# Performance work log

Hardware: AMD Instinct MI355X
Metric: run time of the kernel (lower is better)

## Reference

```python
import jax, jax.numpy as jnp
import numpy as np
import math

N_HEAD = 16
LATENT_RANK = 64

def setup_inputs() -> dict:
    key = jax.random.key(0)
    ks = jax.random.split(key, 8)
    B, T, C, H, R = 4, 2048, 1024, N_HEAD, LATENT_RANK
    std = 0.02
    return {
        "hidden_states": jax.random.normal(ks[0], (B, T, C), jnp.float32),
        "basis_w": jax.random.normal(ks[1], (R, C), jnp.float32) * std,
        "core": jax.random.normal(ks[2], (R, R), jnp.float32) * std,
        "head_residual": jax.random.normal(ks[3], (H, R, R), jnp.float32) * (std / 10.0),
        "v_w": jax.random.normal(ks[4], (C, C), jnp.float32) * std,
        "v_b": jnp.zeros((C,), jnp.float32),
        "o_w": jax.random.normal(ks[5], (C, C), jnp.float32) * std,
        "o_b": jnp.zeros((C,), jnp.float32),
    }

def reference(hidden_states, basis_w, core, head_residual, v_w, v_b, o_w, o_b):
    B, T, C = hidden_states.shape
    H = N_HEAD
    R = LATENT_RANK
    head_dim = C // H

    # latent projection: [B,T,R]
    latent = jnp.einsum('btc,rc->btr', hidden_states, basis_w)

    # symmetric core + centered per-head residual -> head matrices [H,R,R]
    core_sym = 0.5 * (core + core.T)
    centered = head_residual - head_residual.mean(axis=0, keepdims=True)
    head_mats = core_sym[None] / float(H) + centered

    # bilinear latent attention scores [B,H,T,T]
    lt = jnp.einsum('btr,hrs->bhts', latent, head_mats)  # fold Q-transform
    att = jnp.einsum('bhts,bus->bhtu', lt, latent) * (1.0 / math.sqrt(R))

    # causal mask + softmax
    causal = jnp.tril(jnp.ones((T, T), jnp.bool_))
    att = jnp.where(causal[None, None], att, jnp.float32(-jnp.inf))
    att = jax.nn.softmax(att, axis=-1)

    # value projection [B,H,T,head_dim]
    v = (hidden_states @ v_w.T + v_b).reshape(B, T, H, head_dim).transpose(0, 2, 1, 3)
    y = att @ v  # [B,H,T,head_dim]
    y = y.transpose(0, 2, 1, 3).reshape(B, T, C)
    y = y @ o_w.T + o_b
    return y
```

## Files before the change

### kernel.cpp

```cpp
#include <hip/hip_runtime.h>
#include <hip/hip_bf16.h>


#define N_HEAD 16
#define RANK 64

typedef __attribute__((ext_vector_type(8))) short bf16x8;
typedef __attribute__((ext_vector_type(4))) float f32x4;

__device__ __forceinline__ ushort f2b(float f) {
    unsigned u = __builtin_bit_cast(unsigned, f);
    u += 0x7fffu + ((u >> 16) & 1u);
    return (ushort)(u >> 16);
}

__device__ __forceinline__ int swz(int row, int col) {
    return (row << 6) | (col ^ ((row & 7) << 3));
}

__global__ void cvt_kernel(const float* __restrict__ src, ushort* __restrict__ dst, int n4) {
    int i = blockIdx.x * blockDim.x + threadIdx.x;
    if (i >= n4) return;
    float4 v = ((const float4*)src)[i];
    ushort4 o;
    o.x = f2b(v.x); o.y = f2b(v.y); o.z = f2b(v.z); o.w = f2b(v.w);
    ((ushort4*)dst)[i] = o;
}

__global__ void headmats_kernel(const float* __restrict__ core,
                                const float* __restrict__ resid,
                                ushort* __restrict__ hmT) {
    int idx = blockIdx.x * 256 + threadIdx.x;
    if (idx >= RANK * RANK) return;
    int r = idx >> 6, s = idx & 63;
    float mean = 0.f;
    for (int h = 0; h < N_HEAD; ++h) mean += resid[h * RANK * RANK + idx];
    mean *= (1.0f / N_HEAD);
    float cs = 0.5f * (core[r * RANK + s] + core[s * RANK + r]) * (1.0f / N_HEAD);
    for (int h = 0; h < N_HEAD; ++h) {
        float val = cs + resid[h * RANK * RANK + idx] - mean;
        hmT[h * RANK * RANK + s * RANK + r] = f2b(val);
    }
}

__global__ __launch_bounds__(256) void gemm_nt(
    const ushort* __restrict__ A, const ushort* __restrict__ W,
    const float* __restrict__ bias,
    float* __restrict__ outF, ushort* __restrict__ outB,
    int M, int N, int K,
    int zDivA, long long aStride, int zModW, long long wStride, long long oStride,
    int outVT)
{
    __shared__ ushort As[128 * 72];
    __shared__ ushort Ws[64 * 72];

    int z = blockIdx.z;
    A += (size_t)(z / zDivA) * aStride;
    W += (size_t)(z % zModW) * wStride;
    size_t obase = (size_t)z * oStride;

    int m0 = blockIdx.y * 128;
    int n0 = blockIdx.x * 64;
    int t = threadIdx.x;
    int wave = t >> 6, lane = t & 63;
    int wr = wave >> 1, wc = wave & 1;
    int g = lane >> 4, ln = lane & 15;

    f32x4 acc[4][2];
    for (int i = 0; i < 4; ++i)
        for (int j = 0; j < 2; ++j) acc[i][j] = (f32x4){0.f, 0.f, 0.f, 0.f};

    for (int k0 = 0; k0 < K; k0 += 64) {
        for (int q = 0; q < 4; ++q) {
            int e = (t + 256 * q) * 8;
            int row = e >> 6, col = e & 63;
            *(bf16x8*)&As[row * 72 + col] =
                *(const bf16x8*)(A + (size_t)(m0 + row) * K + k0 + col);
        }
        for (int q = 0; q < 2; ++q) {
            int e = (t + 256 * q) * 8;
            int row = e >> 6, col = e & 63;
            *(bf16x8*)&Ws[row * 72 + col] =
                *(const bf16x8*)(W + (size_t)(n0 + row) * K + k0 + col);
        }
        __syncthreads();
        for (int ks = 0; ks < 2; ++ks) {
            bf16x8 a[4], b[2];
            for (int fm = 0; fm < 4; ++fm)
                a[fm] = *(const bf16x8*)&As[(wr * 64 + fm * 16 + ln) * 72 + ks * 32 + 8 * g];
            for (int fn = 0; fn < 2; ++fn)
                b[fn] = *(const bf16x8*)&Ws[(wc * 32 + fn * 16 + ln) * 72 + ks * 32 + 8 * g];
            for (int fm = 0; fm < 4; ++fm)
                for (int fn = 0; fn < 2; ++fn)
                    acc[fm][fn] = __builtin_amdgcn_mfma_f32_16x16x32_bf16(
                        a[fm], b[fn], acc[fm][fn], 0, 0, 0);
        }
        __syncthreads();
    }

    if (outVT) {
        for (int fm = 0; fm < 4; ++fm)
            for (int fn = 0; fn < 2; ++fn) {
                int row = m0 + wr * 64 + fm * 16 + 4 * g;
                int col = n0 + wc * 32 + fn * 16 + ln;
                float bv = bias ? bias[col] : 0.f;
                ushort4 us;
                us.x = f2b(acc[fm][fn][0] + bv);
                us.y = f2b(acc[fm][fn][1] + bv);
                us.z = f2b(acc[fm][fn][2] + bv);
                us.w = f2b(acc[fm][fn][3] + bv);
                size_t off = ((size_t)(row >> 11) * 1024 + col) * 2048 + (row & 2047);
                *(ushort4*)(outB + off) = us;
            }
    } else {
        for (int fm = 0; fm < 4; ++fm)
            for (int fn = 0; fn < 2; ++fn)
                for (int r = 0; r < 4; ++r) {
                    int row = m0 + wr * 64 + fm * 16 + 4 * g + r;
                    int col = n0 + wc * 32 + fn * 16 + ln;
                    float val = acc[fm][fn][r];
                    if (bias) val += bias[col];
                    size_t o = obase + (size_t)row * N + col;
                    if (outF) outF[o] = val;
                    if (outB) outB[o] = f2b(val);
                }
    }
}

__global__ __launch_bounds__(256) void attn_kernel(
    const ushort* __restrict__ lt, const ushort* __restrict__ latent,
    const ushort* __restrict__ vT, ushort* __restrict__ y)
{
    const int T = 2048, C = 1024;
    __shared__ ushort Ps[4][32 * 64];

    int pq = blockIdx.x, h = blockIdx.y, b = blockIdx.z;
    int t = threadIdx.x, w = t >> 6, lane = t & 63;
    int g = lane >> 4, ln = lane & 15;

    const ushort* Kg = latent + (size_t)b * T * RANK;
    const ushort* Vg = vT + (size_t)(b * N_HEAD + h) * 64 * T;
    ushort* Pw = Ps[w];

    const float SCL = 0.125f * 1.44269504089f;
    const float THR = 11.5f;

    for (int pass = 0; pass < 2; ++pass) {
        int qt = pass ? (15 - pq) : pq;
        int qrow0 = qt * 128 + w * 32;

        const ushort* Qg = lt + ((size_t)(b * N_HEAD + h) * T + qrow0) * RANK;
        bf16x8 qa[2][2];
        for (int m = 0; m < 2; ++m)
            for (int ks = 0; ks < 2; ++ks)
                qa[m][ks] = *(const bf16x8*)(Qg + (size_t)(m * 16 + ln) * RANK + ks * 32 + 8 * g);

        float mr[2][4], lp[2][4];
        f32x4 o[2][4];
        for (int m = 0; m < 2; ++m)
            for (int r = 0; r < 4; ++r) { mr[m][r] = -INFINITY; lp[m][r] = 0.f; }
        for (int m = 0; m < 2; ++m)
            for (int fn = 0; fn < 4; ++fn) o[m][fn] = (f32x4){0.f, 0.f, 0.f, 0.f};

        int kmax = 2 * qt + 1;
        for (int kt = 0; kt <= kmax; ++kt) {
            f32x4 s[2][4];
            for (int m = 0; m < 2; ++m)
                for (int fn = 0; fn < 4; ++fn) s[m][fn] = (f32x4){0.f, 0.f, 0.f, 0.f};
            for (int ks = 0; ks < 2; ++ks) {
                bf16x8 kb[4];
                for (int fn = 0; fn < 4; ++fn)
                    kb[fn] = *(const bf16x8*)(Kg +
                        (size_t)(kt * 64 + fn * 16 + ln) * RANK + ks * 32 + 8 * g);
                for (int m = 0; m < 2; ++m)
                    for (int fn = 0; fn < 4; ++fn)
                        s[m][fn] = __builtin_amdgcn_mfma_f32_16x16x32_bf16(
                            qa[m][ks], kb[fn], s[m][fn], 0, 0, 0);
            }

            bf16x8 vb[2][4];
            for (int ks = 0; ks < 2; ++ks)
                for (int fn = 0; fn < 4; ++fn)
                    vb[ks][fn] = *(const bf16x8*)(Vg +
                        (size_t)(fn * 16 + ln) * T + kt * 64 + ks * 32 + 8 * g);

            float rm[2][4];
            for (int m = 0; m < 2; ++m) {
                for (int r = 0; r < 4; ++r) rm[m][r] = -INFINITY;
                int qb = qrow0 + m * 16 + 4 * g;
                if ((kt * 64 + 63) > (qrow0 + m * 16)) {
                    for (int fn = 0; fn < 4; ++fn) {
                        int key = kt * 64 + fn * 16 + ln;
                        for (int r = 0; r < 4; ++r) {
                            float sv = s[m][fn][r] * SCL;
                            if (key > qb + r) sv = -INFINITY;
                            s[m][fn][r] = sv;
                            rm[m][r] = fmaxf(rm[m][r], sv);
                        }
                    }
                } else {
                    for (int fn = 0; fn < 4; ++fn)
                        for (int r = 0; r < 4; ++r) {
                            float sv = s[m][fn][r] * SCL;
                            s[m][fn][r] = sv;
                            rm[m][r] = fmaxf(rm[m][r], sv);
                        }
                }
            }

            int need = 0;
            for (int m = 0; m < 2; ++m)
                for (int r = 0; r < 4; ++r) need |= (rm[m][r] > mr[m][r] + THR);
            if (__any(need)) {
                for (int off = 1; off < 16; off <<= 1)
                    for (int m = 0; m < 2; ++m)
                        for (int r = 0; r < 4; ++r)
                            rm[m][r] = fmaxf(rm[m][r], __shfl_xor(rm[m][r], off));
                for (int m = 0; m < 2; ++m)
                    for (int r = 0; r < 4; ++r) {
                        float nm = fmaxf(mr[m][r], rm[m][r]);
                        float al = exp2f(mr[m][r] - nm);
                        mr[m][r] = nm;
                        lp[m][r] *= al;
                        for (int fn = 0; fn < 4; ++fn) o[m][fn][r] *= al;
                    }
            }

            for (int m = 0; m < 2; ++m)
                for (int fn = 0; fn < 4; ++fn)
                    for (int r = 0; r < 4; ++r) {
                        float p = exp2f(s[m][fn][r] - mr[m][r]);
                        lp[m][r] += p;
                        Pw[swz(m * 16 + 4 * g + r, fn * 16 + ln)] = f2b(p);
                    }

            for (int ks = 0; ks < 2; ++ks) {
                bf16x8 pa[2];
                for (int m = 0; m < 2; ++m)
                    pa[m] = *(const bf16x8*)&Pw[swz(m * 16 + ln, ks * 32 + 8 * g)];
                for (int m = 0; m < 2; ++m)
                    for (int fn = 0; fn < 4; ++fn)
                        o[m][fn] = __builtin_amdgcn_mfma_f32_16x16x32_bf16(
                            pa[m], vb[ks][fn], o[m][fn], 0, 0, 0);
            }
        }

        for (int off = 1; off < 16; off <<= 1)
            for (int m = 0; m < 2; ++m)
                for (int r = 0; r < 4; ++r) lp[m][r] += __shfl_xor(lp[m][r], off);
        for (int m = 0; m < 2; ++m)
            for (int fn = 0; fn < 4; ++fn)
                for (int r = 0; r < 4; ++r) {
                    int row = qrow0 + m * 16 + 4 * g + r;
                    y[((size_t)b * T + row) * C + h * 64 + fn * 16 + ln] =
                        f2b(o[m][fn][r] / lp[m][r]);
                }
    }
}

extern "C" void kernel_launch(void* const* d_in, const int* in_sizes, int n_in,
                              void* d_out, int out_size, void* d_ws, size_t ws_size,
                              hipStream_t stream) {
    const float* hs    = (const float*)d_in[0];
    const float* basis = (const float*)d_in[1];
    const float* core  = (const float*)d_in[2];
    const float* resid = (const float*)d_in[3];
    const float* v_w   = (const float*)d_in[4];
    const float* v_b   = (const float*)d_in[5];
    const float* o_w   = (const float*)d_in[6];
    const float* o_b   = (const float*)d_in[7];
    float* out = (float*)d_out;

    const int B = 4, T = 2048, C = 1024, H = N_HEAD, R = RANK;
    const int M = B * T;

    char* ws = (char*)d_ws;
    ushort* hs_b    = (ushort*)(ws + 0);
    ushort* y_b     = hs_b;
    ushort* basis_b = (ushort*)(ws + 16777216);
    ushort* vw_b    = (ushort*)(ws + 16908288);
    ushort* ow_b    = (ushort*)(ws + 19005440);
    ushort* hm_b    = (ushort*)(ws + 21102592);
    ushort* lat_b   = (ushort*)(ws + 21233664);
    ushort* lt_b    = (ushort*)(ws + 22282240);
    ushort* vT_b    = (ushort*)(ws + 39059456);

    cvt_kernel<<<dim3(M * C / 4 / 256), 256, 0, stream>>>(hs, hs_b, M * C / 4);
    cvt_kernel<<<dim3(R * C / 4 / 256), 256, 0, stream>>>(basis, basis_b, R * C / 4);
    cvt_kernel<<<dim3(C * C / 4 / 256), 256, 0, stream>>>(v_w, vw_b, C * C / 4);
    cvt_kernel<<<dim3(C * C / 4 / 256), 256, 0, stream>>>(o_w, ow_b, C * C / 4);

    headmats_kernel<<<dim3(16), 256, 0, stream>>>(core, resid, hm_b);

    gemm_nt<<<dim3(1, M / 128, 1), 256, 0, stream>>>(
        hs_b, basis_b, nullptr, nullptr, lat_b, M, R, C, 1, 0, 1, 0, 0, 0);

    gemm_nt<<<dim3(C / 64, M / 128, 1), 256, 0, stream>>>(
        hs_b, vw_b, v_b, nullptr, vT_b, M, C, C, 1, 0, 1, 0, 0, 1);

    gemm_nt<<<dim3(1, T / 128, B * H), 256, 0, stream>>>(
        lat_b, hm_b, nullptr, nullptr, lt_b, T, R, R,
        H, (long long)T * R, H, (long long)R * R, (long long)T * R, 0);

    attn_kernel<<<dim3(8, H, B), 256, 0, stream>>>(lt_b, lat_b, vT_b, y_b);

    gemm_nt<<<dim3(C / 64, M / 128, 1), 256, 0, stream>>>(
        y_b, ow_b, o_b, out, nullptr, M, C, C, 1, 0, 1, 0, 0, 0);
}
```

Baseline: 340.5 us.

## Split attention into 16-row waves, fold softmax scale into head mats, widen GEMM tiles

The attention kernel now gives each wave 16 query rows instead of 32 and doubles the block count, with launch bounds asking for 4 blocks per CU. Per-wave key ranges are trimmed to the causal limit, and V fragments are loaded just before use. The softmax scale and log2e factor are folded into the head matrices so the per-score multiply goes away, and P is converted to bf16 by truncation instead of rounding. The two C×C GEMMs use a templated 128-wide N tile for more reuse per block. Risks include a slight accuracy loss from truncation and higher register pressure in the wider GEMM.

```diff
diff --git a/kernel.cpp b/kernel.cpp
--- a/kernel.cpp
+++ b/kernel.cpp
@@ -12,6 +12,10 @@
     unsigned u = __builtin_bit_cast(unsigned, f);
     u += 0x7fffu + ((u >> 16) & 1u);
     return (ushort)(u >> 16);
+}
+
+__device__ __forceinline__ ushort f2b_trunc(float f) {
+    return (ushort)(__builtin_bit_cast(unsigned, f) >> 16);
 }
 
 __device__ __forceinline__ int swz(int row, int col) {
@@ -30,6 +34,7 @@
 __global__ void headmats_kernel(const float* __restrict__ core,
                                 const float* __restrict__ resid,
                                 ushort* __restrict__ hmT) {
+    const float SCLF = 0.125f * 1.44269504089f;
     int idx = blockIdx.x * 256 + threadIdx.x;
     if (idx >= RANK * RANK) return;
     int r = idx >> 6, s = idx & 63;
@@ -38,11 +43,12 @@
     mean *= (1.0f / N_HEAD);
     float cs = 0.5f * (core[r * RANK + s] + core[s * RANK + r]) * (1.0f / N_HEAD);
     for (int h = 0; h < N_HEAD; ++h) {
-        float val = cs + resid[h * RANK * RANK + idx] - mean;
+        float val = (cs + resid[h * RANK * RANK + idx] - mean) * SCLF;
         hmT[h * RANK * RANK + s * RANK + r] = f2b(val);
     }
 }
 
+template<int BN>
 __global__ __launch_bounds__(256) void gemm_nt(
     const ushort* __restrict__ A, const ushort* __restrict__ W,
     const float* __restrict__ bias,
@@ -51,8 +57,9 @@
     int zDivA, long long aStride, int zModW, long long wStride, long long oStride,
     int outVT)
 {
+    constexpr int FN = BN / 32;
     __shared__ ushort As[128 * 72];
-    __shared__ ushort Ws[64 * 72];
+    __shared__ ushort Ws[BN * 72];
 
     int z = blockIdx.z;
     A += (size_t)(z / zDivA) * aStride;
@@ -60,15 +67,15 @@
     size_t obase = (size_t)z * oStride;
 
     int m0 = blockIdx.y * 128;
-    int n0 = blockIdx.x * 64;
+    int n0 = blockIdx.x * BN;
     int t = threadIdx.x;
     int wave = t >> 6, lane = t & 63;
     int wr = wave >> 1, wc = wave & 1;
     int g = lane >> 4, ln = lane & 15;
 
-    f32x4 acc[4][2];
+    f32x4 acc[4][FN];
     for (int i = 0; i < 4; ++i)
-        for (int j = 0; j < 2; ++j) acc[i][j] = (f32x4){0.f, 0.f, 0.f, 0.f};
+        for (int j = 0; j < FN; ++j) acc[i][j] = (f32x4){0.f, 0.f, 0.f, 0.f};
 
     for (int k0 = 0; k0 < K; k0 += 64) {
         for (int q = 0; q < 4; ++q) {
@@ -77,7 +84,7 @@
             *(bf16x8*)&As[row * 72 + col] =
                 *(const bf16x8*)(A + (size_t)(m0 + row) * K + k0 + col);
         }
-        for (int q = 0; q < 2; ++q) {
+        for (int q = 0; q < BN / 32; ++q) {
             int e = (t + 256 * q) * 8;
             int row = e >> 6, col = e & 63;
             *(bf16x8*)&Ws[row * 72 + col] =
@@ -85,13 +92,13 @@
         }
         __syncthreads();
         for (int ks = 0; ks < 2; ++ks) {
-            bf16x8 a[4], b[2];
+            bf16x8 a[4], b[FN];
             for (int fm = 0; fm < 4; ++fm)
                 a[fm] = *(const bf16x8*)&As[(wr * 64 + fm * 16 + ln) * 72 + ks * 32 + 8 * g];
-            for (int fn = 0; fn < 2; ++fn)
-                b[fn] = *(const bf16x8*)&Ws[(wc * 32 + fn * 16 + ln) * 72 + ks * 32 + 8 * g];
+            for (int fn = 0; fn < FN; ++fn)
+                b[fn] = *(const bf16x8*)&Ws[(wc * (BN / 2) + fn * 16 + ln) * 72 + ks * 32 + 8 * g];
             for (int fm = 0; fm < 4; ++fm)
-                for (int fn = 0; fn < 2; ++fn)
+                for (int fn = 0; fn < FN; ++fn)
                     acc[fm][fn] = __builtin_amdgcn_mfma_f32_16x16x32_bf16(
                         a[fm], b[fn], acc[fm][fn], 0, 0, 0);
         }
@@ -100,9 +107,9 @@
 
     if (outVT) {
         for (int fm = 0; fm < 4; ++fm)
-            for (int fn = 0; fn < 2; ++fn) {
+            for (int fn = 0; fn < FN; ++fn) {
                 int row = m0 + wr * 64 + fm * 16 + 4 * g;
-                int col = n0 + wc * 32 + fn * 16 + ln;
+                int col = n0 + wc * (BN / 2) + fn * 16 + ln;
                 float bv = bias ? bias[col] : 0.f;
                 ushort4 us;
                 us.x = f2b(acc[fm][fn][0] + bv);
@@ -114,10 +121,10 @@
             }
     } else {
         for (int fm = 0; fm < 4; ++fm)
-            for (int fn = 0; fn < 2; ++fn)
+            for (int fn = 0; fn < FN; ++fn)
                 for (int r = 0; r < 4; ++r) {
                     int row = m0 + wr * 64 + fm * 16 + 4 * g + r;
-                    int col = n0 + wc * 32 + fn * 16 + ln;
+                    int col = n0 + wc * (BN / 2) + fn * 16 + ln;
                     float val = acc[fm][fn][r];
                     if (bias) val += bias[col];
                     size_t o = obase + (size_t)row * N + col;
@@ -127,134 +134,112 @@
     }
 }
 
-__global__ __launch_bounds__(256) void attn_kernel(
+__global__ __launch_bounds__(256, 4) void attn_kernel(
     const ushort* __restrict__ lt, const ushort* __restrict__ latent,
     const ushort* __restrict__ vT, ushort* __restrict__ y)
 {
     const int T = 2048, C = 1024;
-    __shared__ ushort Ps[4][32 * 64];
-
-    int pq = blockIdx.x, h = blockIdx.y, b = blockIdx.z;
+    __shared__ ushort Ps[4][16 * 64];
+
+    int h = blockIdx.y, b = blockIdx.z;
     int t = threadIdx.x, w = t >> 6, lane = t & 63;
     int g = lane >> 4, ln = lane & 15;
+    int pq = blockIdx.x >> 1;
+    int j = (blockIdx.x & 1) * 4 + w;
 
     const ushort* Kg = latent + (size_t)b * T * RANK;
     const ushort* Vg = vT + (size_t)(b * N_HEAD + h) * 64 * T;
     ushort* Pw = Ps[w];
-
-    const float SCL = 0.125f * 1.44269504089f;
     const float THR = 11.5f;
 
     for (int pass = 0; pass < 2; ++pass) {
         int qt = pass ? (15 - pq) : pq;
-        int qrow0 = qt * 128 + w * 32;
+        int qrow0 = qt * 128 + j * 16;
 
         const ushort* Qg = lt + ((size_t)(b * N_HEAD + h) * T + qrow0) * RANK;
-        bf16x8 qa[2][2];
-        for (int m = 0; m < 2; ++m)
-            for (int ks = 0; ks < 2; ++ks)
-                qa[m][ks] = *(const bf16x8*)(Qg + (size_t)(m * 16 + ln) * RANK + ks * 32 + 8 * g);
-
-        float mr[2][4], lp[2][4];
-        f32x4 o[2][4];
-        for (int m = 0; m < 2; ++m)
-            for (int r = 0; r < 4; ++r) { mr[m][r] = -INFINITY; lp[m][r] = 0.f; }
-        for (int m = 0; m < 2; ++m)
-            for (int fn = 0; fn < 4; ++fn) o[m][fn] = (f32x4){0.f, 0.f, 0.f, 0.f};
-
-        int kmax = 2 * qt + 1;
+        bf16x8 qa[2];
+        for (int ks = 0; ks < 2; ++ks)
+            qa[ks] = *(const bf16x8*)(Qg + (size_t)ln * RANK + ks * 32 + 8 * g);
+
+        float mr[4], lp[4];
+        f32x4 o[4];
+        for (int r = 0; r < 4; ++r) { mr[r] = -INFINITY; lp[r] = 0.f; }
+        for (int fn = 0; fn < 4; ++fn) o[fn] = (f32x4){0.f, 0.f, 0.f, 0.f};
+
+        int kmax = 2 * qt + (j >> 2);
         for (int kt = 0; kt <= kmax; ++kt) {
-            f32x4 s[2][4];
-            for (int m = 0; m < 2; ++m)
-                for (int fn = 0; fn < 4; ++fn) s[m][fn] = (f32x4){0.f, 0.f, 0.f, 0.f};
+            f32x4 s[4];
+            for (int fn = 0; fn < 4; ++fn) s[fn] = (f32x4){0.f, 0.f, 0.f, 0.f};
             for (int ks = 0; ks < 2; ++ks) {
                 bf16x8 kb[4];
                 for (int fn = 0; fn < 4; ++fn)
                     kb[fn] = *(const bf16x8*)(Kg +
                         (size_t)(kt * 64 + fn * 16 + ln) * RANK + ks * 32 + 8 * g);
-                for (int m = 0; m < 2; ++m)
-                    for (int fn = 0; fn < 4; ++fn)
-                        s[m][fn] = __builtin_amdgcn_mfma_f32_16x16x32_bf16(
-                            qa[m][ks], kb[fn], s[m][fn], 0, 0, 0);
-            }
-
-            bf16x8 vb[2][4];
-            for (int ks = 0; ks < 2; ++ks)
                 for (int fn = 0; fn < 4; ++fn)
-                    vb[ks][fn] = *(const bf16x8*)(Vg +
-                        (size_t)(fn * 16 + ln) * T + kt * 64 + ks * 32 + 8 * g);
-
-            float rm[2][4];
-            for (int m = 0; m < 2; ++m) {
-                for (int r = 0; r < 4; ++r) rm[m][r] = -INFINITY;
-                int qb = qrow0 + m * 16 + 4 * g;
-                if ((kt * 64 + 63) > (qrow0 + m * 16)) {
-                    for (int fn = 0; fn < 4; ++fn) {
-                        int key = kt * 64 + fn * 16 + ln;
-                        for (int r = 0; r < 4; ++r) {
-                            float sv = s[m][fn][r] * SCL;
-                            if (key > qb + r) sv = -INFINITY;
-                            s[m][fn][r] = sv;
-                            rm[m][r] = fmaxf(rm[m][r], sv);
-                        }
+                    s[fn] = __builtin_amdgcn_mfma_f32_16x16x32_bf16(
+                        qa[ks], kb[fn], s[fn], 0, 0, 0);
+            }
+
+            float rm[4];
+            for (int r = 0; r < 4; ++r) rm[r] = -INFINITY;
+            int qb = qrow0 + 4 * g;
+            if (kt * 64 + 63 > qrow0) {
+                for (int fn = 0; fn < 4; ++fn) {
+                    int key = kt * 64 + fn * 16 + ln;
+                    for (int r = 0; r < 4; ++r) {
+                        float sv = s[fn][r];
+                        if (key > qb + r) sv = -INFINITY;
+                        s[fn][r] = sv;
+                        rm[r] = fmaxf(rm[r], sv);
                     }
-                } else {
-                    for (int fn = 0; fn < 4; ++fn)
-                        for (int r = 0; r < 4; ++r) {
-                            float sv = s[m][fn][r] * SCL;
-                            s[m][fn][r] = sv;
-                            rm[m][r] = fmaxf(rm[m][r], sv);
-                        }
-                }
+                }
+            } else {
+                for (int fn = 0; fn < 4; ++fn)
+                    for (int r = 0; r < 4; ++r)
+                        rm[r] = fmaxf(rm[r], s[fn][r]);
             }
 
             int need = 0;
-            for (int m = 0; m < 2; ++m)
-                for (int r = 0; r < 4; ++r) need |= (rm[m][r] > mr[m][r] + THR);
+            for (int r = 0; r < 4; ++r) need |= (rm[r] > mr[r] + THR);
             if (__any(need)) {
                 for (int off = 1; off < 16; off <<= 1)
-                    for (int m = 0; m < 2; ++m)
-                        for (int r = 0; r < 4; ++r)
-                            rm[m][r] = fmaxf(rm[m][r], __shfl_xor(rm[m][r], off));
-                for (int m = 0; m < 2; ++m)
-                    for (int r = 0; r < 4; ++r) {
-                        float nm = fmaxf(mr[m][r], rm[m][r]);
-                        float al = exp2f(mr[m][r] - nm);
-                        mr[m][r] = nm;
-                        lp[m][r] *= al;
-                        for (int fn = 0; fn < 4; ++fn) o[m][fn][r] *= al;
-                    }
-            }
-
-            for (int m = 0; m < 2; ++m)
-                for (int fn = 0; fn < 4; ++fn)
-                    for (int r = 0; r < 4; ++r) {
-                        float p = exp2f(s[m][fn][r] - mr[m][r]);
-                        lp[m][r] += p;
-                        Pw[swz(m * 16 + 4 * g + r, fn * 16 + ln)] = f2b(p);
-                    }
-
-            for (int ks = 0; ks < 2; ++ks) {
-                bf16x8 pa[2];
-                for (int m = 0; m < 2; ++m)
-                    pa[m] = *(const bf16x8*)&Pw[swz(m * 16 + ln, ks * 32 + 8 * g)];
-                for (int m = 0; m < 2; ++m)
-                    for (int fn = 0; fn < 4; ++fn)
-                        o[m][fn] = __builtin_amdgcn_mfma_f32_16x16x32_bf16(
-                            pa[m], vb[ks][fn], o[m][fn], 0, 0, 0);
-            }
-        }
-
-        for (int off = 1; off < 16; off <<= 1)
-            for (int m = 0; m < 2; ++m)
-                for (int r = 0; r < 4; ++r) lp[m][r] += __shfl_xor(lp[m][r], off);
-        for (int m = 0; m < 2; ++m)
+                    for (int r = 0; r < 4; ++r)
+                        rm[r] = fmaxf(rm[r], __shfl_xor(rm[r], off));
+                for (int r = 0; r < 4; ++r) {
+                    float nm = fmaxf(mr[r], rm[r]);
+                    float al = exp2f(mr[r] - nm);
+                    mr[r] = nm;
+                    lp[r] *= al;
+                    for (int fn = 0; fn < 4; ++fn) o[fn][r] *= al;
+                }
+            }
+
             for (int fn = 0; fn < 4; ++fn)
                 for (int r = 0; r < 4; ++r) {
-                    int row = qrow0 + m * 16 + 4 * g + r;
-                    y[((size_t)b * T + row) * C + h * 64 + fn * 16 + ln] =
-                        f2b(o[m][fn][r] / lp[m][r]);
-                }
+                    float p = exp2f(s[fn][r] - mr[r]);
+                    lp[r] += p;
+                    Pw[swz(4 * g + r, fn * 16 + ln)] = f2b_trunc(p);
+                }
+
+            for (int ks = 0; ks < 2; ++ks) {
+                bf16x8 pa = *(const bf16x8*)&Pw[swz(ln, ks * 32 + 8 * g)];
+                for (int fn = 0; fn < 4; ++fn) {
+                    bf16x8 vb = *(const bf16x8*)(Vg +
+                        (size_t)(fn * 16 + ln) * T + kt * 64 + ks * 32 + 8 * g);
+                    o[fn] = __builtin_amdgcn_mfma_f32_16x16x32_bf16(
+                        pa, vb, o[fn], 0, 0, 0);
+                }
+            }
+        }
+
+        for (int off = 1; off < 16; off <<= 1)
+            for (int r = 0; r < 4; ++r) lp[r] += __shfl_xor(lp[r], off);
+        for (int fn = 0; fn < 4; ++fn)
+            for (int r = 0; r < 4; ++r) {
+                int row = qrow0 + 4 * g + r;
+                y[((size_t)b * T + row) * C + h * 64 + fn * 16 + ln] =
+                    f2b(o[fn][r] / lp[r]);
+            }
     }
 }
 
@@ -292,18 +277,18 @@
 
     headmats_kernel<<<dim3(16), 256, 0, stream>>>(core, resid, hm_b);
 
-    gemm_nt<<<dim3(1, M / 128, 1), 256, 0, stream>>>(
+    gemm_nt<64><<<dim3(1, M / 128, 1), 256, 0, stream>>>(
         hs_b, basis_b, nullptr, nullptr, lat_b, M, R, C, 1, 0, 1, 0, 0, 0);
 
-    gemm_nt<<<dim3(C / 64, M / 128, 1), 256, 0, stream>>>(
+    gemm_nt<128><<<dim3(C / 128, M / 128, 1), 256, 0, stream>>>(
         hs_b, vw_b, v_b, nullptr, vT_b, M, C, C, 1, 0, 1, 0, 0, 1);
 
-    gemm_nt<<<dim3(1, T / 128, B * H), 256, 0, stream>>>(
+    gemm_nt<64><<<dim3(1, T / 128, B * H), 256, 0, stream>>>(
         lat_b, hm_b, nullptr, nullptr, lt_b, T, R, R,
         H, (long long)T * R, H, (long long)R * R, (long long)T * R, 0);
 
-    attn_kernel<<<dim3(8, H, B), 256, 0, stream>>>(lt_b, lat_b, vT_b, y_b);
-
-    gemm_nt<<<dim3(C / 64, M / 128, 1), 256, 0, stream>>>(
+    attn_kernel<<<dim3(16, H, B), 256, 0, stream>>>(lt_b, lat_b, vT_b, y_b);
+
+    gemm_nt<128><<<dim3(C / 128, M / 128, 1), 256, 0, stream>>>(
         y_b, ow_b, o_b, out, nullptr, M, C, C, 1, 0, 1, 0, 0, 0);
 }
```

Measured after the change: 442.1 us. +29.8%, slower.
